# Kernel optimization log

Hardware: AMD Instinct MI355X
Metric: run time of the kernel (lower is better)

The kernel has to match this reference:

```python
import jax, jax.numpy as jnp
import numpy as np

NUM_LAYERS = 6
D_MODEL = 256
N_HEADS = 8
N_LEVELS = 4
N_POINTS = 4
D_FFN = 1024
HEAD_DIM = D_MODEL // N_HEADS
B = 2
NQ = 1600
SPATIAL = np.array([[64, 64], [32, 32], [16, 16], [8, 8]], dtype=np.int64)  # (H_l, W_l)
LEVEL_START = np.concatenate([[0], np.cumsum(SPATIAL.prod(1))[:-1]]).astype(np.int64)
S_TOTAL = int(SPATIAL.prod(1).sum())  # 5440


def layer_norm(x, g, b, eps=1e-5):
    mu = x.mean(-1, keepdims=True)
    var = ((x - mu) ** 2).mean(-1, keepdims=True)
    return (x - mu) * jax.lax.rsqrt(var + eps) * g + b


def mha(q, k, v, wq, bq, wk, bk, wv, bv, wo, bo):
    # torch nn.MultiheadAttention math (dropout=eval identity)
    Bb, N, d = q.shape
    def proj(x, w, bias):
        return (x @ w.T + bias).reshape(Bb, -1, N_HEADS, HEAD_DIM).transpose(0, 2, 1, 3)
    qh, kh, vh = proj(q, wq, bq), proj(k, wk, bk), proj(v, wv, bv)
    scores = jnp.einsum('bhqd,bhkd->bhqk', qh, kh) / np.float32(np.sqrt(HEAD_DIM))
    attn = jax.nn.softmax(scores, axis=-1)
    out = jnp.einsum('bhqk,bhkd->bhqd', attn, vh).transpose(0, 2, 1, 3).reshape(Bb, N, d)
    return out @ wo.T + bo


def ms_deform_attn(query, ref_points, src, w_off, b_off, w_attn, b_attn, w_val, b_val, w_out, b_out):
    Bb, Nq, d = query.shape
    value = (src @ w_val.T + b_val).reshape(Bb, -1, N_HEADS, HEAD_DIM)  # [B,S,H,D]
    off = (query @ w_off.T + b_off).reshape(Bb, Nq, N_HEADS, N_LEVELS, N_POINTS, 2)
    aw = (query @ w_attn.T + b_attn).reshape(Bb, Nq, N_HEADS, N_LEVELS * N_POINTS)
    aw = jax.nn.softmax(aw, -1).reshape(Bb, Nq, N_HEADS, N_LEVELS, N_POINTS)
    # offset normalizer is (W_l, H_l)
    norm = jnp.asarray(SPATIAL[:, ::-1].copy(), dtype=query.dtype)  # [L,2]
    loc = ref_points[:, :, None, :, None, :] + off / norm[None, None, None, :, None, :]
    out = jnp.zeros((Bb, Nq, N_HEADS, HEAD_DIM), query.dtype)
    for l in range(N_LEVELS):
        Hl, Wl = int(SPATIAL[l, 0]), int(SPATIAL[l, 1])
        s0 = int(LEVEL_START[l])
        v_l = value[:, s0:s0 + Hl * Wl].transpose(0, 2, 1, 3)  # [B,H,S_l,D]
        loc_l = loc[:, :, :, l]  # [B,Nq,H,P,2]
        # grid_sample bilinear, align_corners=False, padding zeros
        x = loc_l[..., 0] * Wl - 0.5
        y = loc_l[..., 1] * Hl - 0.5
        x0 = jnp.floor(x)
        y0 = jnp.floor(y)
        wx1 = x - x0
        wy1 = y - y0
        samp = jnp.zeros((Bb, Nq, N_HEADS, N_POINTS, HEAD_DIM), query.dtype)
        for dy, wy in ((0, 1.0 - wy1), (1, wy1)):
            for dx, wx in ((0, 1.0 - wx1), (1, wx1)):
                xi = x0 + dx
                yi = y0 + dy
                valid = ((xi >= 0) & (xi <= Wl - 1) & (yi >= 0) & (yi <= Hl - 1)).astype(query.dtype)
                xi_c = jnp.clip(xi, 0, Wl - 1).astype(jnp.int32)
                yi_c = jnp.clip(yi, 0, Hl - 1).astype(jnp.int32)
                idx = (yi_c * Wl + xi_c).transpose(0, 2, 1, 3).reshape(Bb, N_HEADS, Nq * N_POINTS)
                g = jnp.take_along_axis(v_l, idx[..., None], axis=2)  # [B,H,Nq*P,D]
                g = g.reshape(Bb, N_HEADS, Nq, N_POINTS, HEAD_DIM).transpose(0, 2, 1, 3, 4)
                samp = samp + g * (wx * wy * valid)[..., None]
        out = out + (samp * aw[:, :, :, l, :, None]).sum(3)
    return out.reshape(Bb, Nq, d) @ w_out.T + b_out


def decoder_forward(tgt, query_pos, reference_points, src, params):
    out = tgt
    for i in range(NUM_LAYERS):
        p = {k: v[i] for k, v in params.items()}
        q = out + query_pos
        t2 = mha(q, q, out, p['sa_w_q'], p['sa_b_q'], p['sa_w_k'], p['sa_b_k'],
                 p['sa_w_v'], p['sa_b_v'], p['sa_w_o'], p['sa_b_o'])
        out = layer_norm(out + t2, p['ln2_g'], p['ln2_b'])
        t2 = ms_deform_attn(out + query_pos, reference_points, src,
                            p['ca_w_off'], p['ca_b_off'], p['ca_w_attn'], p['ca_b_attn'],
                            p['ca_w_val'], p['ca_b_val'], p['ca_w_out'], p['ca_b_out'])
        out = out + t2
        out = layer_norm(out, p['ln1_g'], p['ln1_b'])
        t2 = jax.nn.relu(out @ p['ffn_w1'].T + p['ffn_b1']) @ p['ffn_w2'].T + p['ffn_b2']
        out = layer_norm(out + t2, p['ln3_g'], p['ln3_b'])
    return out


PARAM_NAMES = ['sa_w_q', 'sa_b_q', 'sa_w_k', 'sa_b_k', 'sa_w_v', 'sa_b_v', 'sa_w_o', 'sa_b_o',
               'ln2_g', 'ln2_b',
               'ca_w_off', 'ca_b_off', 'ca_w_attn', 'ca_b_attn', 'ca_w_val', 'ca_b_val',
               'ca_w_out', 'ca_b_out', 'ln1_g', 'ln1_b',
               'ffn_w1', 'ffn_b1', 'ffn_w2', 'ffn_b2', 'ln3_g', 'ln3_b']


def setup_inputs() -> dict:
    key = jax.random.key(0)
    ks = jax.random.split(key, 64)
    d = D_MODEL
    HLP = N_HEADS * N_LEVELS * N_POINTS
    shapes = {
        'sa_w_q': (d, d), 'sa_b_q': (d,), 'sa_w_k': (d, d), 'sa_b_k': (d,),
        'sa_w_v': (d, d), 'sa_b_v': (d,), 'sa_w_o': (d, d), 'sa_b_o': (d,),
        'ca_w_off': (HLP * 2, d), 'ca_b_off': (HLP * 2,),
        'ca_w_attn': (HLP, d), 'ca_b_attn': (HLP,),
        'ca_w_val': (d, d), 'ca_b_val': (d,),
        'ca_w_out': (d, d), 'ca_b_out': (d,),
        'ffn_w1': (D_FFN, d), 'ffn_b1': (D_FFN,),
        'ffn_w2': (d, D_FFN), 'ffn_b2': (D_FFN * 0 + d,) if False else (d,),
    }
    inp = {}
    inp['tgt'] = jax.random.normal(ks[0], (B, NQ, d), jnp.float32)
    inp['query_pos'] = jax.random.normal(ks[1], (B, NQ, d), jnp.float32)
    inp['reference_points'] = jax.random.uniform(ks[2], (B, NQ, N_LEVELS, 2), jnp.float32)
    inp['src'] = jax.random.normal(ks[3], (B, S_TOTAL, d), jnp.float32)
    i = 4
    for name in PARAM_NAMES:
        if name.startswith('ln'):
            if name.endswith('_g'):
                inp[name] = jnp.ones((NUM_LAYERS, d), jnp.float32)
            else:
                inp[name] = jnp.zeros((NUM_LAYERS, d), jnp.float32)
        else:
            shp = (NUM_LAYERS,) + shapes[name]
            inp[name] = jax.random.normal(ks[i], shp, jnp.float32) * 0.02
            i += 1
    inp['src_spatial_shapes'] = jnp.asarray(SPATIAL)
    inp['src_level_start_index'] = jnp.asarray(LEVEL_START)
    return inp


def reference(tgt, query_pos, reference_points, src,
              sa_w_q, sa_b_q, sa_w_k, sa_b_k, sa_w_v, sa_b_v, sa_w_o, sa_b_o,
              ln2_g, ln2_b,
              ca_w_off, ca_b_off, ca_w_attn, ca_b_attn, ca_w_val, ca_b_val,
              ca_w_out, ca_b_out, ln1_g, ln1_b,
              ffn_w1, ffn_b1, ffn_w2, ffn_b2, ln3_g, ln3_b,
              src_spatial_shapes, src_level_start_index):
    params = dict(zip(PARAM_NAMES, (sa_w_q, sa_b_q, sa_w_k, sa_b_k, sa_w_v, sa_b_v, sa_w_o, sa_b_o,
                                    ln2_g, ln2_b, ca_w_off, ca_b_off, ca_w_attn, ca_b_attn,
                                    ca_w_val, ca_b_val, ca_w_out, ca_b_out, ln1_g, ln1_b,
                                    ffn_w1, ffn_b1, ffn_w2, ffn_b2, ln3_g, ln3_b)))
    return decoder_forward(tgt, query_pos, reference_points, src, params)
```

## Files before the change

### kernel.cpp

```cpp
#include <hip/hip_runtime.h>

#define D_MODEL   256
#define NQ        1600
#define BATCH     2
#define NHEAD     8
#define HDIM      32
#define S_TOTAL   5440
#define D_FFN     1024
#define NUM_LAYERS 6

#define M_Q   (BATCH * NQ)
#define M_V   (BATCH * S_TOTAL)
#define ROW_ELEMS ((size_t)M_Q * D_MODEL)

using short8  = __attribute__((ext_vector_type(8))) short;
using short4v = __attribute__((ext_vector_type(4))) short;
using floatx4 = __attribute__((ext_vector_type(4))) float;

#if __has_builtin(__builtin_amdgcn_mfma_f32_16x16x16_bf16)
  #define MFMA16K16(a,b,c) __builtin_amdgcn_mfma_f32_16x16x16_bf16((a),(b),(c),0,0,0)
#else
  #define MFMA16K16(a,b,c) __builtin_amdgcn_mfma_f32_16x16x16bf16_1k((a),(b),(c),0,0,0)
#endif

#if __has_builtin(__builtin_amdgcn_exp2f)
  #define EXP2F(x) __builtin_amdgcn_exp2f(x)
#else
  #define EXP2F(x) exp2f(x)
#endif

__device__ __forceinline__ ushort f2bf(float f) {
    union { float f; unsigned u; } x; x.f = f;
    unsigned r = (x.u + 0x7fffu + ((x.u >> 16) & 1u)) >> 16;
    return (ushort)r;
}
__device__ __forceinline__ ushort f2bf_trunc(float f) {
    union { float f; unsigned u; } x; x.f = f;
    return (ushort)(x.u >> 16);
}
__device__ __forceinline__ float bf2f(ushort b) {
    union { unsigned u; float f; } x; x.u = ((unsigned)b) << 16;
    return x.f;
}

struct GSeg {
    const ushort* A;
    const ushort* W;
    const float*  bias;
    void*         C;
    int           ldc;
    int           mode;
    int           mblk;
    float         scale;
};
struct GArgs { GSeg s[16]; };

__global__ __launch_bounds__(256) void gemm_multi(GArgs args, int K)
{
    const GSeg sg = args.s[blockIdx.y];
    if ((int)blockIdx.x >= sg.mblk) return;
    __shared__ ushort Al[64][40];
    __shared__ ushort Bl[64][40];
    const int tid  = threadIdx.x;
    const int bm   = blockIdx.x * 64;
    const int lr   = tid >> 2;
    const int lc   = tid & 3;
    const int wave = tid >> 6;
    const int lane = tid & 63;
    const int mo   = (wave & 1) * 32;
    const int no   = (wave >> 1) * 32;
    const int row16 = lane & 15;
    const int quad  = lane >> 4;

    floatx4 acc[2][2] = {};

    const ushort* aG = sg.A + (size_t)(bm + lr) * K + lc * 8;
    const ushort* wG = sg.W + (size_t)lr * K + lc * 8;

    for (int k0 = 0; k0 < K; k0 += 32) {
        __syncthreads();
        *(short8*)&Al[lr][lc * 8] = *(const short8*)(aG + k0);
        *(short8*)&Bl[lr][lc * 8] = *(const short8*)(wG + k0);
        __syncthreads();
        short8 af0 = *(const short8*)&Al[mo + row16][quad * 8];
        short8 af1 = *(const short8*)&Al[mo + 16 + row16][quad * 8];
        short8 bf0 = *(const short8*)&Bl[no + row16][quad * 8];
        short8 bf1 = *(const short8*)&Bl[no + 16 + row16][quad * 8];
        acc[0][0] = __builtin_amdgcn_mfma_f32_16x16x32_bf16(af0, bf0, acc[0][0], 0, 0, 0);
        acc[0][1] = __builtin_amdgcn_mfma_f32_16x16x32_bf16(af0, bf1, acc[0][1], 0, 0, 0);
        acc[1][0] = __builtin_amdgcn_mfma_f32_16x16x32_bf16(af1, bf0, acc[1][0], 0, 0, 0);
        acc[1][1] = __builtin_amdgcn_mfma_f32_16x16x32_bf16(af1, bf1, acc[1][1], 0, 0, 0);
    }

#pragma unroll
    for (int mi = 0; mi < 2; ++mi)
#pragma unroll
        for (int ni = 0; ni < 2; ++ni) {
            const int col = no + ni * 16 + row16;
            const float bv = sg.bias[col];
            const int rowb = bm + mo + mi * 16 + quad * 4;
            if (sg.mode == 4) {
                const int b = rowb / NQ;
                const int mloc = rowb - b * NQ;
                ushort* base = (ushort*)sg.C
                    + ((size_t)b * 8 * NQ + (size_t)(col >> 5) * NQ) * 32 + (col & 31);
#pragma unroll
                for (int r = 0; r < 4; ++r)
                    base[(size_t)(mloc + r) * 32] = f2bf((acc[mi][ni][r] + bv) * sg.scale);
            } else if (sg.mode == 5) {
                const int b = rowb / NQ;
                const int mloc = rowb - b * NQ;
                ushort4 st;
                st.x = f2bf((acc[mi][ni][0] + bv) * sg.scale);
                st.y = f2bf((acc[mi][ni][1] + bv) * sg.scale);
                st.z = f2bf((acc[mi][ni][2] + bv) * sg.scale);
                st.w = f2bf((acc[mi][ni][3] + bv) * sg.scale);
                ushort* base = (ushort*)sg.C
                    + ((size_t)b * 8 * NQ + (size_t)(col >> 5) * NQ) * 32;
                *(ushort4*)(base + ((size_t)(mloc >> 2) * 32 + (col & 31)) * 4) = st;
            } else {
#pragma unroll
                for (int r = 0; r < 4; ++r) {
                    const int row = rowb + r;
                    float v = (acc[mi][ni][r] + bv) * sg.scale;
                    if (sg.mode == 0)
                        ((float*)sg.C)[(size_t)row * sg.ldc + col] = v;
                    else if (sg.mode == 1)
                        ((ushort*)sg.C)[(size_t)row * sg.ldc + col] = f2bf(fmaxf(v, 0.f));
                    else
                        ((ushort*)sg.C)[(size_t)row * sg.ldc + col] = f2bf(v);
                }
            }
        }
}

#define FSHIFT 16.0f

__global__ __launch_bounds__(256) void attn_mfma(const ushort* __restrict__ Qh,
                                                 const ushort* __restrict__ Kh,
                                                 const ushort* __restrict__ Vt,
                                                 ushort* __restrict__ Oh)
{
    const int bh = blockIdx.x;
    const int h  = bh & 7, b = bh >> 3;
    const int q0 = blockIdx.y * 16;
    const int tid  = threadIdx.x;
    const int wave = tid >> 6, lane = tid & 63;
    const int lr   = lane & 15, quad = lane >> 4;

    __shared__ float Ol[4][16][33];
    __shared__ float Ll[4][16];

    const ushort* Qb = Qh + (size_t)bh * NQ * 32;
    const ushort* Kb = Kh + (size_t)bh * NQ * 32;
    const ushort* Vb = Vt + (size_t)bh * NQ * 32;

    const short8 qf = *(const short8*)(Qb + (size_t)(q0 + lr) * 32 + quad * 8);

    float lsum = 0.f;
    floatx4 accO[2] = {};
    const floatx4 zero = {0.f, 0.f, 0.f, 0.f};

    const int NT = NQ / 64;
    for (int t = wave; t < NT; t += 4) {
        const int k0 = t * 64;
#pragma unroll
        for (int cb = 0; cb < 4; ++cb) {
            const short8 kf = *(const short8*)(Kb + (size_t)(k0 + cb * 16 + lr) * 32 + quad * 8);
            const floatx4 st = __builtin_amdgcn_mfma_f32_16x16x32_bf16(kf, qf, zero, 0, 0, 0);
            const short4v v0 = *(const short4v*)(Vb + (size_t)(k0 + cb * 16 + quad * 4) * 32 + lr * 4);
            const short4v v1 = *(const short4v*)(Vb + (size_t)(k0 + cb * 16 + quad * 4) * 32 + 64 + lr * 4);
            short4v pf;
#pragma unroll
            for (int r = 0; r < 4; ++r) {
                const float p = EXP2F(fminf(st[r], 100.f) - FSHIFT);
                lsum += p;
                pf[r] = (short)f2bf_trunc(p);
            }
            accO[0] = MFMA16K16(pf, v0, accO[0]);
            accO[1] = MFMA16K16(pf, v1, accO[1]);
        }
    }

    lsum += __shfl_xor(lsum, 16);
    lsum += __shfl_xor(lsum, 32);
    if (quad == 0) Ll[wave][lr] = lsum;
#pragma unroll
    for (int r = 0; r < 4; ++r) {
        const int q = quad * 4 + r;
        Ol[wave][q][lr]      = accO[0][r];
        Ol[wave][q][16 + lr] = accO[1][r];
    }
    __syncthreads();

#pragma unroll
    for (int i = 0; i < 2; ++i) {
        const int idx = tid + i * 256;
        const int q = idx >> 5, d = idx & 31;
        const float o  = Ol[0][q][d] + Ol[1][q][d] + Ol[2][q][d] + Ol[3][q][d];
        const float lt = Ll[0][q] + Ll[1][q] + Ll[2][q] + Ll[3][q];
        Oh[(size_t)(b * NQ + q0 + q) * 256 + h * 32 + d] = f2bf(o / lt);
    }
}

struct CvtSeg { const float* in; ushort* out; int n4; };
struct CvtArgs { CvtSeg seg[11]; };

__global__ __launch_bounds__(256) void convert_kernel(CvtArgs args)
{
    const CvtSeg sg = args.seg[blockIdx.y];
    const int i = blockIdx.x * 256 + threadIdx.x;
    if (i < sg.n4) {
        float4 v = ((const float4*)sg.in)[i];
        ushort4 o;
        o.x = f2bf(v.x); o.y = f2bf(v.y); o.z = f2bf(v.z); o.w = f2bf(v.w);
        ((ushort4*)sg.out)[i] = o;
    }
}

__global__ __launch_bounds__(256) void init_out_kernel(const float* __restrict__ tgt,
                                                       const float* __restrict__ qpos,
                                                       float* __restrict__ out,
                                                       ushort* __restrict__ out_h,
                                                       ushort* __restrict__ qadd_h, int n4)
{
    const int i = blockIdx.x * 256 + threadIdx.x;
    if (i < n4) {
        float4 v = ((const float4*)tgt)[i];
        float4 p = ((const float4*)qpos)[i];
        ((float4*)out)[i] = v;
        ushort4 o, qa;
        o.x = f2bf(v.x); o.y = f2bf(v.y); o.z = f2bf(v.z); o.w = f2bf(v.w);
        qa.x = f2bf(v.x + p.x); qa.y = f2bf(v.y + p.y);
        qa.z = f2bf(v.z + p.z); qa.w = f2bf(v.w + p.w);
        ((ushort4*)out_h)[i] = o;
        ((ushort4*)qadd_h)[i] = qa;
    }
}

__global__ __launch_bounds__(256) void residual_ln_kernel(const float* __restrict__ x,
                                                          const float* __restrict__ t2,
                                                          const float* __restrict__ g,
                                                          const float* __restrict__ bt,
                                                          const float* __restrict__ qpos,
                                                          float* __restrict__ outp,
                                                          ushort* __restrict__ outp_h,
                                                          ushort* __restrict__ qadd_h)
{
    const int row = blockIdx.x;
    const int c = threadIdx.x;
    const size_t idx = (size_t)row * D_MODEL + c;
    float v = x[idx] + t2[idx];

    float s = v, s2 = v * v;
#pragma unroll
    for (int off = 32; off; off >>= 1) {
        s  += __shfl_xor(s,  off);
        s2 += __shfl_xor(s2, off);
    }
    __shared__ float ws[4], ws2[4];
    const int wid = c >> 6;
    if ((c & 63) == 0) { ws[wid] = s; ws2[wid] = s2; }
    __syncthreads();
    const float tot  = ws[0] + ws[1] + ws[2] + ws[3];
    const float tot2 = ws2[0] + ws2[1] + ws2[2] + ws2[3];
    const float mu  = tot * (1.f / 256.f);
    const float var = tot2 * (1.f / 256.f) - mu * mu;
    const float r = (v - mu) * rsqrtf(var + 1e-5f) * g[c] + bt[c];
    outp[idx] = r;
    outp_h[idx] = f2bf(r);
    qadd_h[idx] = f2bf(r + qpos[idx]);
}

__global__ __launch_bounds__(256) void sample_kernel(const ushort* __restrict__ value,
                                                     const float* __restrict__ off,
                                                     const float* __restrict__ aw,
                                                     const float* __restrict__ ref,
                                                     ushort* __restrict__ outp_h)
{
    const int bq = blockIdx.x;
    const int b  = bq / NQ;
    const int h  = threadIdx.x >> 5;
    const int c  = threadIdx.x & 31;

    const float* offrow = off + (size_t)bq * 256 + h * 32;
    const float* awrow  = aw  + (size_t)bq * 128 + h * 16;
    const float* refrow = ref + (size_t)bq * 8;

    float w16[16];
    {
        float mx = -1e30f;
#pragma unroll
        for (int i = 0; i < 16; ++i) { w16[i] = awrow[i]; mx = fmaxf(mx, w16[i]); }
        float sum = 0.f;
#pragma unroll
        for (int i = 0; i < 16; ++i) { w16[i] = __expf(w16[i] - mx); sum += w16[i]; }
        const float inv = 1.f / sum;
#pragma unroll
        for (int i = 0; i < 16; ++i) w16[i] *= inv;
    }

    const int HL[4]  = {64, 32, 16, 8};
    const int WLv[4] = {64, 32, 16, 8};
    const int S0[4]  = {0, 4096, 5120, 5376};

    float acc = 0.f;
#pragma unroll
    for (int l = 0; l < 4; ++l) {
        const int Hl = HL[l], Wl = WLv[l];
        const float rx = refrow[l * 2 + 0];
        const float ry = refrow[l * 2 + 1];
        const size_t lvl_base = ((size_t)b * S_TOTAL + S0[l]);
#pragma unroll
        for (int p = 0; p < 4; ++p) {
            const float ox = offrow[l * 8 + p * 2 + 0];
            const float oy = offrow[l * 8 + p * 2 + 1];
            const float w  = w16[l * 4 + p];
            const float locx = rx + ox / (float)Wl;
            const float locy = ry + oy / (float)Hl;
            const float x = locx * (float)Wl - 0.5f;
            const float y = locy * (float)Hl - 0.5f;
            const float x0f = floorf(x), y0f = floorf(y);
            const float wx1 = x - x0f, wy1 = y - y0f;
            const int x0 = (int)x0f, y0 = (int)y0f;
#pragma unroll
            for (int dy = 0; dy < 2; ++dy) {
                const int yi = y0 + dy;
                const float wy = dy ? wy1 : (1.f - wy1);
                const bool vy = (yi >= 0) && (yi <= Hl - 1);
                const int yc = min(max(yi, 0), Hl - 1);
#pragma unroll
                for (int dx = 0; dx < 2; ++dx) {
                    const int xi = x0 + dx;
                    const float wx = dx ? wx1 : (1.f - wx1);
                    const bool vx = (xi >= 0) && (xi <= Wl - 1);
                    const int xc = min(max(xi, 0), Wl - 1);
                    const float gv = bf2f(value[((lvl_base + (size_t)yc * Wl + xc)) * 256 + h * 32 + c]);
                    acc += (vx && vy) ? gv * (wx * wy * w) : 0.f;
                }
            }
        }
    }
    outp_h[(size_t)bq * D_MODEL + h * 32 + c] = f2bf(acc);
}

extern "C" void kernel_launch(void* const* d_in, const int* in_sizes, int n_in,
                              void* d_out, int out_size, void* d_ws, size_t ws_size,
                              hipStream_t stream)
{
    const float* tgt  = (const float*)d_in[0];
    const float* qpos = (const float*)d_in[1];
    const float* refp = (const float*)d_in[2];
    const float* src  = (const float*)d_in[3];

    float* bufT   = (float*)d_ws;
    float* bufOff = bufT   + ROW_ELEMS;
    float* bufAw  = bufOff + ROW_ELEMS;

    ushort* out_h   = (ushort*)(bufAw + (size_t)M_Q * 128);
    ushort* qadd_h  = out_h   + ROW_ELEMS;
    ushort* bufX_h  = qadd_h  + ROW_ELEMS;
    ushort* bufQh   = bufX_h  + ROW_ELEMS;
    ushort* bufKh   = bufQh   + ROW_ELEMS;
    ushort* bufVt   = bufKh   + ROW_ELEMS;
    ushort* bufF_h  = bufVt   + ROW_ELEMS;
    ushort* bufVal  = bufF_h  + (size_t)M_Q * D_FFN;
    ushort* src_h   = bufVal  + (size_t)M_V * D_MODEL;
    ushort* wpool   = src_h   + (size_t)M_V * D_MODEL;

    ushort* wq_h    = wpool;
    ushort* wk_h    = wq_h    + 393216;
    ushort* wv_h    = wk_h    + 393216;
    ushort* wo_h    = wv_h    + 393216;
    ushort* woff_h  = wo_h    + 393216;
    ushort* wattn_h = woff_h  + 393216;
    ushort* wval_h  = wattn_h + 196608;
    ushort* wout_h  = wval_h  + 393216;
    ushort* w1_h    = wout_h  + 393216;
    ushort* w2_h    = w1_h    + 1572864;

    float* out = (float*)d_out;

    CvtArgs ca;
    ca.seg[0]  = { src,                    src_h,   (int)((size_t)M_V * D_MODEL / 4) };
    ca.seg[1]  = { (const float*)d_in[4],  wq_h,    393216 / 4 };
    ca.seg[2]  = { (const float*)d_in[6],  wk_h,    393216 / 4 };
    ca.seg[3]  = { (const float*)d_in[8],  wv_h,    393216 / 4 };
    ca.seg[4]  = { (const float*)d_in[10], wo_h,    393216 / 4 };
    ca.seg[5]  = { (const float*)d_in[14], woff_h,  393216 / 4 };
    ca.seg[6]  = { (const float*)d_in[16], wattn_h, 196608 / 4 };
    ca.seg[7]  = { (const float*)d_in[18], wval_h,  393216 / 4 };
    ca.seg[8]  = { (const float*)d_in[20], wout_h,  393216 / 4 };
    ca.seg[9]  = { (const float*)d_in[24], w1_h,    1572864 / 4 };
    ca.seg[10] = { (const float*)d_in[26], w2_h,    1572864 / 4 };
    convert_kernel<<<dim3(2720, 11), 256, 0, stream>>>(ca);

    init_out_kernel<<<800, 256, 0, stream>>>(tgt, qpos, out, out_h, qadd_h, (int)(ROW_ELEMS / 4));

    const float QSCALE = 0.1767766952966369f * 1.4426950408889634f;
    const int MB_Q = M_Q / 64;
    const int MB_V = M_V / 64;

    for (int l = 0; l < NUM_LAYERS; ++l) {
        const float* sa_b_q    = (const float*)d_in[5]  + (size_t)l * 256;
        const float* sa_b_k    = (const float*)d_in[7]  + (size_t)l * 256;
        const float* sa_b_v    = (const float*)d_in[9]  + (size_t)l * 256;
        const float* sa_b_o    = (const float*)d_in[11] + (size_t)l * 256;
        const float* ln2_g     = (const float*)d_in[12] + (size_t)l * 256;
        const float* ln2_b     = (const float*)d_in[13] + (size_t)l * 256;
        const float* ca_b_off  = (const float*)d_in[15] + (size_t)l * 256;
        const float* ca_b_attn = (const float*)d_in[17] + (size_t)l * 128;
        const float* ca_b_val  = (const float*)d_in[19] + (size_t)l * 256;
        const float* ca_b_out  = (const float*)d_in[21] + (size_t)l * 256;
        const float* ln1_g     = (const float*)d_in[22] + (size_t)l * 256;
        const float* ln1_b     = (const float*)d_in[23] + (size_t)l * 256;
        const float* ffn_b1    = (const float*)d_in[25] + (size_t)l * 1024;
        const float* ffn_b2    = (const float*)d_in[27] + (size_t)l * 256;
        const float* ln3_g     = (const float*)d_in[28] + (size_t)l * 256;
        const float* ln3_b     = (const float*)d_in[29] + (size_t)l * 256;

        const ushort* wq = wq_h    + (size_t)l * 65536;
        const ushort* wk = wk_h    + (size_t)l * 65536;
        const ushort* wv = wv_h    + (size_t)l * 65536;
        const ushort* wo = wo_h    + (size_t)l * 65536;
        const ushort* wf = woff_h  + (size_t)l * 65536;
        const ushort* wa = wattn_h + (size_t)l * 32768;
        const ushort* wl = wval_h  + (size_t)l * 65536;
        const ushort* wu = wout_h  + (size_t)l * 65536;
        const ushort* w1 = w1_h    + (size_t)l * 262144;
        const ushort* w2 = w2_h    + (size_t)l * 262144;

        GArgs ga;

        for (int i = 0; i < 4; ++i) {
            ga.s[i]      = { qadd_h, wq + (size_t)i * 64 * 256, sa_b_q + i * 64,
                             bufQh + (size_t)(2 * i) * NQ * 32, 0, 4, MB_Q, QSCALE };
            ga.s[4 + i]  = { qadd_h, wk + (size_t)i * 64 * 256, sa_b_k + i * 64,
                             bufKh + (size_t)(2 * i) * NQ * 32, 0, 4, MB_Q, 1.f };
            ga.s[8 + i]  = { out_h,  wv + (size_t)i * 64 * 256, sa_b_v + i * 64,
                             bufVt + (size_t)(2 * i) * NQ * 32, 0, 5, MB_Q, 1.f };
            ga.s[12 + i] = { src_h,  wl + (size_t)i * 64 * 256, ca_b_val + i * 64,
                             bufVal + i * 64, 256, 2, MB_V, 1.f };
        }
        gemm_multi<<<dim3(MB_V, 16), 256, 0, stream>>>(ga, 256);

        attn_mfma<<<dim3(16, NQ / 16), 256, 0, stream>>>(bufQh, bufKh, bufVt, bufX_h);

        for (int i = 0; i < 4; ++i)
            ga.s[i] = { bufX_h, wo + (size_t)i * 64 * 256, sa_b_o + i * 64, bufT + i * 64, 256, 0, MB_Q, 1.f };
        gemm_multi<<<dim3(MB_Q, 4), 256, 0, stream>>>(ga, 256);

        residual_ln_kernel<<<M_Q, 256, 0, stream>>>(out, bufT, ln2_g, ln2_b, qpos, out, out_h, qadd_h);

        for (int i = 0; i < 4; ++i)
            ga.s[i] = { qadd_h, wf + (size_t)i * 64 * 256, ca_b_off + i * 64, bufOff + i * 64, 256, 0, MB_Q, 1.f };
        for (int i = 0; i < 2; ++i)
            ga.s[4 + i] = { qadd_h, wa + (size_t)i * 64 * 256, ca_b_attn + i * 64, bufAw + i * 64, 128, 0, MB_Q, 1.f };
        gemm_multi<<<dim3(MB_Q, 6), 256, 0, stream>>>(ga, 256);

        sample_kernel<<<M_Q, 256, 0, stream>>>(bufVal, bufOff, bufAw, refp, bufX_h);

        for (int i = 0; i < 4; ++i)
            ga.s[i] = { bufX_h, wu + (size_t)i * 64 * 256, ca_b_out + i * 64, bufT + i * 64, 256, 0, MB_Q, 1.f };
        gemm_multi<<<dim3(MB_Q, 4), 256, 0, stream>>>(ga, 256);

        residual_ln_kernel<<<M_Q, 256, 0, stream>>>(out, bufT, ln1_g, ln1_b, qpos, out, out_h, qadd_h);

        for (int i = 0; i < 16; ++i)
            ga.s[i] = { out_h, w1 + (size_t)i * 64 * 256, ffn_b1 + i * 64, bufF_h + i * 64, 1024, 1, MB_Q, 1.f };
        gemm_multi<<<dim3(MB_Q, 16), 256, 0, stream>>>(ga, 256);

        for (int i = 0; i < 4; ++i)
            ga.s[i] = { bufF_h, w2 + (size_t)i * 64 * 1024, ffn_b2 + i * 64, bufT + i * 64, 256, 0, MB_Q, 1.f };
        gemm_multi<<<dim3(MB_Q, 4), 256, 0, stream>>>(ga, 1024);

        residual_ln_kernel<<<M_Q, 256, 0, stream>>>(out, bufT, ln3_g, ln3_b, qpos, out, out_h, qadd_h);
    }

    (void)in_sizes; (void)n_in; (void)out_size; (void)ws_size;
}
```

Measured before the change: 903.3 us.

## Hoist value projections of all layers into one batched GEMM; widen attention query tile

The cross-attention value projection depends only on src and the per-layer weights, so all six layers' projections now run in a single up-front gemm_multi launch into a per-layer value buffer. Each layer's QKV GEMM launch then covers only MB_Q row blocks instead of MB_V, with no idle blocks. Separately, the self-attention kernel now handles 32 queries per block, so each K/V load is reused across two query tiles. The changes cost six times the value-buffer workspace plus more registers and shared memory in the attention kernel.

New measurement: 873.8 us. 1.03x faster.

```diff
diff --git a/kernel.cpp b/kernel.cpp
--- a/kernel.cpp
+++ b/kernel.cpp
@@ -53,7 +53,7 @@
     int           mblk;
     float         scale;
 };
-struct GArgs { GSeg s[16]; };
+struct GArgs { GSeg s[24]; };
 
 __global__ __launch_bounds__(256) void gemm_multi(GArgs args, int K)
 {
@@ -143,22 +143,23 @@
 {
     const int bh = blockIdx.x;
     const int h  = bh & 7, b = bh >> 3;
-    const int q0 = blockIdx.y * 16;
+    const int q0 = blockIdx.y * 32;
     const int tid  = threadIdx.x;
     const int wave = tid >> 6, lane = tid & 63;
     const int lr   = lane & 15, quad = lane >> 4;
 
-    __shared__ float Ol[4][16][33];
-    __shared__ float Ll[4][16];
+    __shared__ float Ol[4][32][33];
+    __shared__ float Ll[4][32];
 
     const ushort* Qb = Qh + (size_t)bh * NQ * 32;
     const ushort* Kb = Kh + (size_t)bh * NQ * 32;
     const ushort* Vb = Vt + (size_t)bh * NQ * 32;
 
-    const short8 qf = *(const short8*)(Qb + (size_t)(q0 + lr) * 32 + quad * 8);
-
-    float lsum = 0.f;
-    floatx4 accO[2] = {};
+    const short8 qfA = *(const short8*)(Qb + (size_t)(q0 + lr) * 32 + quad * 8);
+    const short8 qfB = *(const short8*)(Qb + (size_t)(q0 + 16 + lr) * 32 + quad * 8);
+
+    float lsumA = 0.f, lsumB = 0.f;
+    floatx4 accOA[2] = {}, accOB[2] = {};
     const floatx4 zero = {0.f, 0.f, 0.f, 0.f};
 
     const int NT = NQ / 64;
@@ -167,34 +168,41 @@
 #pragma unroll
         for (int cb = 0; cb < 4; ++cb) {
             const short8 kf = *(const short8*)(Kb + (size_t)(k0 + cb * 16 + lr) * 32 + quad * 8);
-            const floatx4 st = __builtin_amdgcn_mfma_f32_16x16x32_bf16(kf, qf, zero, 0, 0, 0);
+            const floatx4 stA = __builtin_amdgcn_mfma_f32_16x16x32_bf16(kf, qfA, zero, 0, 0, 0);
+            const floatx4 stB = __builtin_amdgcn_mfma_f32_16x16x32_bf16(kf, qfB, zero, 0, 0, 0);
             const short4v v0 = *(const short4v*)(Vb + (size_t)(k0 + cb * 16 + quad * 4) * 32 + lr * 4);
             const short4v v1 = *(const short4v*)(Vb + (size_t)(k0 + cb * 16 + quad * 4) * 32 + 64 + lr * 4);
-            short4v pf;
+            short4v pfA, pfB;
 #pragma unroll
             for (int r = 0; r < 4; ++r) {
-                const float p = EXP2F(fminf(st[r], 100.f) - FSHIFT);
-                lsum += p;
-                pf[r] = (short)f2bf_trunc(p);
+                const float pA = EXP2F(fminf(stA[r], 100.f) - FSHIFT);
+                const float pB = EXP2F(fminf(stB[r], 100.f) - FSHIFT);
+                lsumA += pA; lsumB += pB;
+                pfA[r] = (short)f2bf_trunc(pA);
+                pfB[r] = (short)f2bf_trunc(pB);
             }
-            accO[0] = MFMA16K16(pf, v0, accO[0]);
-            accO[1] = MFMA16K16(pf, v1, accO[1]);
+            accOA[0] = MFMA16K16(pfA, v0, accOA[0]);
+            accOA[1] = MFMA16K16(pfA, v1, accOA[1]);
+            accOB[0] = MFMA16K16(pfB, v0, accOB[0]);
+            accOB[1] = MFMA16K16(pfB, v1, accOB[1]);
         }
     }
 
-    lsum += __shfl_xor(lsum, 16);
-    lsum += __shfl_xor(lsum, 32);
-    if (quad == 0) Ll[wave][lr] = lsum;
+    lsumA += __shfl_xor(lsumA, 16);  lsumB += __shfl_xor(lsumB, 16);
+    lsumA += __shfl_xor(lsumA, 32);  lsumB += __shfl_xor(lsumB, 32);
+    if (quad == 0) { Ll[wave][lr] = lsumA; Ll[wave][16 + lr] = lsumB; }
 #pragma unroll
     for (int r = 0; r < 4; ++r) {
         const int q = quad * 4 + r;
-        Ol[wave][q][lr]      = accO[0][r];
-        Ol[wave][q][16 + lr] = accO[1][r];
+        Ol[wave][q][lr]           = accOA[0][r];
+        Ol[wave][q][16 + lr]      = accOA[1][r];
+        Ol[wave][16 + q][lr]      = accOB[0][r];
+        Ol[wave][16 + q][16 + lr] = accOB[1][r];
     }
     __syncthreads();
 
 #pragma unroll
-    for (int i = 0; i < 2; ++i) {
+    for (int i = 0; i < 4; ++i) {
         const int idx = tid + i * 256;
         const int q = idx >> 5, d = idx & 31;
         const float o  = Ol[0][q][d] + Ol[1][q][d] + Ol[2][q][d] + Ol[3][q][d];
@@ -365,7 +373,7 @@
     ushort* bufVt   = bufKh   + ROW_ELEMS;
     ushort* bufF_h  = bufVt   + ROW_ELEMS;
     ushort* bufVal  = bufF_h  + (size_t)M_Q * D_FFN;
-    ushort* src_h   = bufVal  + (size_t)M_V * D_MODEL;
+    ushort* src_h   = bufVal  + (size_t)NUM_LAYERS * M_V * D_MODEL;
     ushort* wpool   = src_h   + (size_t)M_V * D_MODEL;
 
     ushort* wq_h    = wpool;
@@ -401,6 +409,19 @@
     const int MB_Q = M_Q / 64;
     const int MB_V = M_V / 64;
 
+    {
+        GArgs gv;
+        for (int l = 0; l < NUM_LAYERS; ++l) {
+            const ushort* wl = wval_h + (size_t)l * 65536;
+            const float* bv  = (const float*)d_in[19] + (size_t)l * 256;
+            ushort* dst = bufVal + (size_t)l * M_V * D_MODEL;
+            for (int i = 0; i < 4; ++i)
+                gv.s[l * 4 + i] = { src_h, wl + (size_t)i * 64 * 256, bv + i * 64,
+                                    dst + i * 64, 256, 2, MB_V, 1.f };
+        }
+        gemm_multi<<<dim3(MB_V, 24), 256, 0, stream>>>(gv, 256);
+    }
+
     for (int l = 0; l < NUM_LAYERS; ++l) {
         const float* sa_b_q    = (const float*)d_in[5]  + (size_t)l * 256;
         const float* sa_b_k    = (const float*)d_in[7]  + (size_t)l * 256;
@@ -410,7 +431,6 @@
         const float* ln2_b     = (const float*)d_in[13] + (size_t)l * 256;
         const float* ca_b_off  = (const float*)d_in[15] + (size_t)l * 256;
         const float* ca_b_attn = (const float*)d_in[17] + (size_t)l * 128;
-        const float* ca_b_val  = (const float*)d_in[19] + (size_t)l * 256;
         const float* ca_b_out  = (const float*)d_in[21] + (size_t)l * 256;
         const float* ln1_g     = (const float*)d_in[22] + (size_t)l * 256;
         const float* ln1_b     = (const float*)d_in[23] + (size_t)l * 256;
@@ -425,26 +445,25 @@
         const ushort* wo = wo_h    + (size_t)l * 65536;
         const ushort* wf = woff_h  + (size_t)l * 65536;
         const ushort* wa = wattn_h + (size_t)l * 32768;
-        const ushort* wl = wval_h  + (size_t)l * 65536;
         const ushort* wu = wout_h  + (size_t)l * 65536;
         const ushort* w1 = w1_h    + (size_t)l * 262144;
         const ushort* w2 = w2_h    + (size_t)l * 262144;
 
+        ushort* valL = bufVal + (size_t)l * M_V * D_MODEL;
+
         GArgs ga;
 
         for (int i = 0; i < 4; ++i) {
-            ga.s[i]      = { qadd_h, wq + (size_t)i * 64 * 256, sa_b_q + i * 64,
-                             bufQh + (size_t)(2 * i) * NQ * 32, 0, 4, MB_Q, QSCALE };
-            ga.s[4 + i]  = { qadd_h, wk + (size_t)i * 64 * 256, sa_b_k + i * 64,
-                             bufKh + (size_t)(2 * i) * NQ * 32, 0, 4, MB_Q, 1.f };
-            ga.s[8 + i]  = { out_h,  wv + (size_t)i * 64 * 256, sa_b_v + i * 64,
-                             bufVt + (size_t)(2 * i) * NQ * 32, 0, 5, MB_Q, 1.f };
-            ga.s[12 + i] = { src_h,  wl + (size_t)i * 64 * 256, ca_b_val + i * 64,
-                             bufVal + i * 64, 256, 2, MB_V, 1.f };
+            ga.s[i]     = { qadd_h, wq + (size_t)i * 64 * 256, sa_b_q + i * 64,
+                            bufQh + (size_t)(2 * i) * NQ * 32, 0, 4, MB_Q, QSCALE };
+            ga.s[4 + i] = { qadd_h, wk + (size_t)i * 64 * 256, sa_b_k + i * 64,
+                            bufKh + (size_t)(2 * i) * NQ * 32, 0, 4, MB_Q, 1.f };
+            ga.s[8 + i] = { out_h,  wv + (size_t)i * 64 * 256, sa_b_v + i * 64,
+                            bufVt + (size_t)(2 * i) * NQ * 32, 0, 5, MB_Q, 1.f };
         }
-        gemm_multi<<<dim3(MB_V, 16), 256, 0, stream>>>(ga, 256);
-
-        attn_mfma<<<dim3(16, NQ / 16), 256, 0, stream>>>(bufQh, bufKh, bufVt, bufX_h);
+        gemm_multi<<<dim3(MB_Q, 12), 256, 0, stream>>>(ga, 256);
+
+        attn_mfma<<<dim3(16, NQ / 32), 256, 0, stream>>>(bufQh, bufKh, bufVt, bufX_h);
 
         for (int i = 0; i < 4; ++i)
             ga.s[i] = { bufX_h, wo + (size_t)i * 64 * 256, sa_b_o + i * 64, bufT + i * 64, 256, 0, MB_Q, 1.f };
@@ -458,7 +477,7 @@
             ga.s[4 + i] = { qadd_h, wa + (size_t)i * 64 * 256, ca_b_attn + i * 64, bufAw + i * 64, 128, 0, MB_Q, 1.f };
         gemm_multi<<<dim3(MB_Q, 6), 256, 0, stream>>>(ga, 256);
 
-        sample_kernel<<<M_Q, 256, 0, stream>>>(bufVal, bufOff, bufAw, refp, bufX_h);
+        sample_kernel<<<M_Q, 256, 0, stream>>>(valL, bufOff, bufAw, refp, bufX_h);
 
         for (int i = 0; i < 4; ++i)
             ga.s[i] = { bufX_h, wu + (size_t)i * 64 * 256, ca_b_out + i * 64, bufT + i * 64, 256, 0, MB_Q, 1.f };
```
